# Performance work log

Measured on AMD Instinct MI355X. Metric: run time of the kernel, lower is better.

## Reference

```python
import jax, jax.numpy as jnp
import numpy as np

N = 100000      # nodes
E = 1600000     # edges (avg degree 16)
F_IN = 512      # input node features
H = 8           # heads in conv1
D = 8           # per-head dim in conv1
C = 7           # classes
NEG_SLOPE = 0.2 # PyG GATConv default leaky_relu slope


def setup_inputs() -> dict:
    key = jax.random.key(0)
    ks = jax.random.split(key, 10)
    s = 0.05
    return {
        "x": jax.random.normal(ks[0], (N, F_IN), jnp.float32),
        "edge_index": jax.random.randint(ks[1], (2, E), 0, N, dtype=jnp.int64),
        "W1": jax.random.normal(ks[2], (F_IN, H * D), jnp.float32) * s,
        "a1_src": jax.random.normal(ks[3], (H, D), jnp.float32) * s,
        "a1_dst": jax.random.normal(ks[4], (H, D), jnp.float32) * s,
        "b1": jnp.zeros((H * D,), jnp.float32),
        "W2": jax.random.normal(ks[5], (H * D, C), jnp.float32) * s,
        "a2_src": jax.random.normal(ks[6], (1, C), jnp.float32) * s,
        "a2_dst": jax.random.normal(ks[7], (1, C), jnp.float32) * s,
        "b2": jnp.zeros((C,), jnp.float32),
    }


def _gat_conv(x, src, dst, W, a_src, a_dst, b, heads, dim, concat, n):
    # linear transform -> [N, H, D]
    h = (x @ W).reshape(n, heads, dim)
    # per-node attention halves: [N, H]
    al_src = jnp.einsum('nhd,hd->nh', h, a_src)
    al_dst = jnp.einsum('nhd,hd->nh', h, a_dst)
    # per-edge logits, leaky relu: [E', H]
    e = jax.nn.leaky_relu(al_src[src] + al_dst[dst], NEG_SLOPE)
    # segment softmax over incoming edges of each dst node
    m = jax.lax.stop_gradient(jax.ops.segment_max(e, dst, num_segments=n))
    p = jnp.exp(e - m[dst])
    z = jax.ops.segment_sum(p, dst, num_segments=n)
    alpha = p / z[dst]                                   # [E', H]
    # weighted scatter-add of source messages -> [N, H, D]
    out = jax.ops.segment_sum(h[src] * alpha[..., None], dst, num_segments=n)
    out = out.reshape(n, heads * dim) if concat else out.mean(axis=1)
    return out + b


def reference(x, edge_index, W1, a1_src, a1_dst, b1, W2, a2_src, a2_dst, b2):
    n = x.shape[0]
    # PyG GATConv default: add self loops
    loops = jnp.arange(n, dtype=edge_index.dtype)
    src = jnp.concatenate([edge_index[0], loops])
    dst = jnp.concatenate([edge_index[1], loops])
    h = _gat_conv(x, src, dst, W1, a1_src, a1_dst, b1, H, D, True, n)
    h = jax.nn.elu(h)
    out = _gat_conv(h, src, dst, W2, a2_src, a2_dst, b2, 1, C, False, n)
    return jax.nn.log_softmax(out, axis=1)
```

## Files before the change

kernel.cpp:

```cpp
#include <hip/hip_runtime.h>
#include <math.h>

#define N_NODES 100000
#define N_EDGES 1600000
#define F_IN 512
#define HD 64
#define CC 7
#define NKT (F_IN / 32)
#define BS 64
#define NBK ((N_NODES + BS - 1) / BS)
#define ECAP 2048
#define SCHUNK 16384
#define SBLK ((N_EDGES + SCHUNK - 1) / SCHUNK)
#define GEMMBLKS ((N_NODES + 63) / 64)
#define W1WORK (NKT * 4 * 64)

typedef __attribute__((ext_vector_type(8))) short short8;
typedef __attribute__((ext_vector_type(4))) float f32x4;

__device__ inline unsigned short f2bf(float f) {
    union { float f; unsigned u; } v; v.f = f;
    unsigned u = v.u;
    return (unsigned short)((u + 0x7fffu + ((u >> 16) & 1u)) >> 16);
}
__device__ inline float bf2f(unsigned short b) {
    union { unsigned u; float f; } v; v.u = ((unsigned)b) << 16;
    return v.f;
}

__global__ __launch_bounds__(256) void prep_kernel(const float* __restrict__ W1,
                                                   unsigned short* __restrict__ wf,
                                                   int* __restrict__ bcur) {
    if (blockIdx.x == 16) {
        for (int i = threadIdx.x; i < NBK; i += 256) bcur[i] = 0;
        return;
    }
    int t = blockIdx.x * 256 + threadIdx.x;
    if (t >= W1WORK) return;
    int lane = t & 63;
    int ct = (t >> 6) & 3;
    int kt = t >> 8;
    int k0 = kt * 32 + (lane >> 4) * 8;
    int col = ct * 16 + (lane & 15);
    unsigned short* dst = wf + (size_t)t * 8;
    #pragma unroll
    for (int j = 0; j < 8; ++j) dst[j] = f2bf(W1[(k0 + j) * HD + col]);
}

__global__ __launch_bounds__(256) void fused_kernel(
        const int* __restrict__ ei, int* __restrict__ bcur, int* __restrict__ pairs,
        const float* __restrict__ x, const unsigned short* __restrict__ wf,
        const float* __restrict__ a1s, const float* __restrict__ a1d,
        unsigned short* __restrict__ h1b, float* __restrict__ als,
        float* __restrict__ ald) {
    __shared__ float ls[64 * 65];
    const int bid = blockIdx.x;
    const int tid = threadIdx.x;
    if (bid < SBLK) {
        int* cnt = (int*)ls;
        int* bas = cnt + NBK;
        const int e0 = bid * SCHUNK;
        int e1 = e0 + SCHUNK; if (e1 > N_EDGES) e1 = N_EDGES;
        for (int b = tid; b < NBK; b += 256) cnt[b] = 0;
        __syncthreads();
        for (int i = e0 + tid; i < e1; i += 256)
            atomicAdd(&cnt[ei[N_EDGES + i] >> 6], 1);
        __syncthreads();
        const int boff = (bid * 263) % NBK;
        for (int bb = tid; bb < NBK; bb += 256) {
            int b = bb + boff; if (b >= NBK) b -= NBK;
            int c = cnt[b];
            bas[b] = c ? atomicAdd(&bcur[b], c) : 0;
            cnt[b] = 0;
        }
        __syncthreads();
        for (int i = e0 + tid; i < e1; i += 256) {
            int s = ei[i];
            int t = ei[N_EDGES + i];
            int b = t >> 6;
            int pos = bas[b] + atomicAdd(&cnt[b], 1);
            if (pos < ECAP) pairs[(size_t)b * ECAP + pos] = (s << 6) | (t & (BS - 1));
        }
        return;
    }
    const int gb = bid - SBLK;
    const int wave = tid >> 6;
    const int lane = tid & 63;
    int arow = gb * 64 + wave * 16 + (lane & 15);
    if (arow >= N_NODES) arow = N_NODES - 1;
    const float* xp = x + (size_t)arow * F_IN + (lane >> 4) * 8;
    const short8* wp = (const short8*)wf;

    f32x4 acc[4] = {};
    #pragma unroll 4
    for (int kt = 0; kt < NKT; ++kt) {
        f32x4 a0 = *(const f32x4*)(xp + kt * 32);
        f32x4 a1 = *(const f32x4*)(xp + kt * 32 + 4);
        union { short8 s; unsigned short u[8]; } af;
        af.u[0] = f2bf(a0.x); af.u[1] = f2bf(a0.y);
        af.u[2] = f2bf(a0.z); af.u[3] = f2bf(a0.w);
        af.u[4] = f2bf(a1.x); af.u[5] = f2bf(a1.y);
        af.u[6] = f2bf(a1.z); af.u[7] = f2bf(a1.w);
        #pragma unroll
        for (int ct = 0; ct < 4; ++ct) {
            short8 bf = wp[kt * 256 + ct * 64 + lane];
            acc[ct] = __builtin_amdgcn_mfma_f32_16x16x32_bf16(af.s, bf, acc[ct], 0, 0, 0);
        }
    }
    const int lrow_base = wave * 16 + (lane >> 4) * 4;
    const int ocol = lane & 15;
    #pragma unroll
    for (int ct = 0; ct < 4; ++ct) {
        #pragma unroll
        for (int r = 0; r < 4; ++r) {
            int lrow = lrow_base + r;
            int orow = gb * 64 + lrow;
            ls[lrow * 65 + ct * 16 + ocol] = acc[ct][r];
            if (orow < N_NODES)
                h1b[(size_t)orow * HD + ct * 16 + ocol] = f2bf(acc[ct][r]);
        }
    }
    __syncthreads();
    #pragma unroll
    for (int task = tid; task < 64 * 8; task += 256) {
        int r = task >> 3, h = task & 7;
        int node = gb * 64 + r;
        if (node < N_NODES) {
            float s = 0.f, d = 0.f;
            #pragma unroll
            for (int k = 0; k < 8; ++k) {
                float v = ls[r * 65 + h * 8 + k];
                s += v * a1s[h * 8 + k];
                d += v * a1d[h * 8 + k];
            }
            als[node * 8 + h] = s;
            ald[node * 8 + h] = d;
        }
    }
}

__global__ __launch_bounds__(256) void sortcsr_kernel(const int* __restrict__ bcur,
                                                      const int* __restrict__ pairs,
                                                      int* __restrict__ csr_src,
                                                      int* __restrict__ rowptr,
                                                      int* __restrict__ rowcnt) {
    __shared__ int cnt[BS];
    __shared__ int start[BS];
    __shared__ int srcl[ECAP];
    const int tid = threadIdx.x;
    const int lane = tid & 63;
    const int n0 = blockIdx.x * BS;
    const size_t bbase = (size_t)blockIdx.x * ECAP;
    const int* bp = pairs + bbase;
    int ne = bcur[blockIdx.x]; if (ne > ECAP) ne = ECAP;
    if (tid < BS) cnt[tid] = 0;
    __syncthreads();
    for (int k = tid; k < ne; k += 256)
        atomicAdd(&cnt[bp[k] & (BS - 1)], 1);
    __syncthreads();
    if (tid < 64) {
        int a = cnt[lane];
        int xx = a;
        #pragma unroll
        for (int o = 1; o < 64; o <<= 1) { int u = __shfl_up(xx, o, 64); if (lane >= o) xx += u; }
        start[lane] = xx - a;
        cnt[lane] = 0;
    }
    __syncthreads();
    for (int k = tid; k < ne; k += 256) {
        int v = bp[k];
        int ln = v & (BS - 1);
        int pos = start[ln] + atomicAdd(&cnt[ln], 1);
        srcl[pos] = v >> 6;
    }
    __syncthreads();
    for (int k = tid; k < ne; k += 256) csr_src[bbase + k] = srcl[k];
    if (tid < BS) {
        int node = n0 + tid;
        if (node < N_NODES) {
            rowptr[node] = (int)bbase + start[tid];
            rowcnt[node] = cnt[tid];
        }
    }
}

__global__ __launch_bounds__(256) void gather1_kernel(
        const int* __restrict__ rowptr, const int* __restrict__ rowcnt,
        const int* __restrict__ csr_src,
        const float* __restrict__ als, const float* __restrict__ ald,
        const unsigned short* __restrict__ h1b, const float* __restrict__ b1,
        const float* __restrict__ W2, const float* __restrict__ a2s,
        const float* __restrict__ a2d,
        unsigned short* __restrict__ g2b, float* __restrict__ al2s,
        float* __restrict__ al2d) {
    int node = (blockIdx.x * 256 + threadIdx.x) >> 6;
    if (node >= N_NODES) return;
    const int lane = threadIdx.x & 63;
    const int h = lane >> 3;
    const int e8 = lane & 7, base8 = lane & 56;
    const int rs = rowptr[node], ncnt = rowcnt[node];
    const float aldt = ald[node * 8 + h];
    float e = als[node * 8 + h] + aldt;
    e = (e >= 0.f) ? e : 0.2f * e;
    float p = __expf(e);
    float acc = p * bf2f(h1b[(size_t)node * HD + lane]);
    float z = p;
    int k = 0;
    for (; k + 8 <= ncnt; k += 8) {
        int s_own = csr_src[rs + k + e8];
        int se[8];
        #pragma unroll
        for (int q = 0; q < 8; ++q) se[q] = __shfl(s_own, base8 | q, 64);
        float ve[8];
        #pragma unroll
        for (int q = 0; q < 8; ++q) ve[q] = bf2f(h1b[(size_t)se[q] * HD + lane]);
        float ee = als[s_own * 8 + h] + aldt;
        ee = (ee >= 0.f) ? ee : 0.2f * ee;
        float pv = __expf(ee);
        #pragma unroll
        for (int q = 0; q < 8; ++q) {
            float pe = __shfl(pv, base8 | q, 64);
            z += pe;
            acc = fmaf(pe, ve[q], acc);
        }
    }
    if (k < ncnt) {
        const int m = ncnt - k;
        int idx = rs + k + ((e8 < m) ? e8 : (m - 1));
        int s_own = csr_src[idx];
        int se[8];
        #pragma unroll
        for (int q = 0; q < 8; ++q) se[q] = __shfl(s_own, base8 | q, 64);
        float ee = als[s_own * 8 + h] + aldt;
        ee = (ee >= 0.f) ? ee : 0.2f * ee;
        float pv = __expf(ee);
        for (int q = 0; q < m; ++q) {
            float pe = __shfl(pv, base8 | q, 64);
            float ve = bf2f(h1b[(size_t)se[q] * HD + lane]);
            z += pe;
            acc = fmaf(pe, ve, acc);
        }
    }
    float v = acc / z + b1[lane];
    v = (v > 0.f) ? v : (__expf(v) - 1.f);
    float w[CC];
    #pragma unroll
    for (int c = 0; c < CC; ++c) w[c] = W2[lane * CC + c];
    float g[CC];
    #pragma unroll
    for (int c = 0; c < CC; ++c) {
        float r = v * w[c];
        #pragma unroll
        for (int d = 1; d < 64; d <<= 1) r += __shfl_xor(r, d, 64);
        g[c] = r;
    }
    float s2 = 0.f, d2 = 0.f;
    #pragma unroll
    for (int c = 0; c < CC; ++c) { s2 += g[c] * a2s[c]; d2 += g[c] * a2d[c]; }
    if (lane < CC) g2b[(size_t)node * 8 + lane] = f2bf(g[lane]);
    if (lane == CC) g2b[(size_t)node * 8 + CC] = 0;
    if (lane == 8) al2s[node] = s2;
    if (lane == 9) al2d[node] = d2;
}

__global__ __launch_bounds__(256) void gather2_kernel(
        const int* __restrict__ rowptr, const int* __restrict__ rowcnt,
        const int* __restrict__ csr_src,
        const float* __restrict__ al2s, const float* __restrict__ al2d,
        const unsigned short* __restrict__ g2b, const float* __restrict__ b2,
        float* __restrict__ out) {
    int gid = blockIdx.x * 256 + threadIdx.x;
    int n = gid >> 3, c = gid & 7;
    if (n >= N_NODES) return;
    const int lane = threadIdx.x & 63;
    const int base8 = lane & 56;
    const int rs = rowptr[n], ncnt = rowcnt[n];
    const float adn = al2d[n];
    float e = al2s[n] + adn;
    e = (e >= 0.f) ? e : 0.2f * e;
    float p = __expf(e);
    float acc = p * bf2f(g2b[(size_t)n * 8 + c]);
    float z = p;
    int k = 0;
    for (; k + 8 <= ncnt; k += 8) {
        int s_own = csr_src[rs + k + c];
        int se[8];
        #pragma unroll
        for (int q = 0; q < 8; ++q) se[q] = __shfl(s_own, base8 | q, 64);
        float ve[8];
        #pragma unroll
        for (int q = 0; q < 8; ++q) ve[q] = bf2f(g2b[(size_t)se[q] * 8 + c]);
        float ee = al2s[s_own] + adn;
        ee = (ee >= 0.f) ? ee : 0.2f * ee;
        float pv = __expf(ee);
        #pragma unroll
        for (int q = 0; q < 8; ++q) {
            float pe = __shfl(pv, base8 | q, 64);
            z += pe;
            acc = fmaf(pe, ve[q], acc);
        }
    }
    if (k < ncnt) {
        const int m = ncnt - k;
        int idx = rs + k + ((c < m) ? c : (m - 1));
        int s_own = csr_src[idx];
        int se[8];
        #pragma unroll
        for (int q = 0; q < 8; ++q) se[q] = __shfl(s_own, base8 | q, 64);
        float ee = al2s[s_own] + adn;
        ee = (ee >= 0.f) ? ee : 0.2f * ee;
        float pv = __expf(ee);
        for (int q = 0; q < m; ++q) {
            float pe = __shfl(pv, base8 | q, 64);
            float ve = bf2f(g2b[(size_t)se[q] * 8 + c]);
            z += pe;
            acc = fmaf(pe, ve, acc);
        }
    }
    float o = (c < CC) ? (acc / z + b2[c]) : -1e30f;
    float m2 = o;
    #pragma unroll
    for (int d = 1; d < 8; d <<= 1) m2 = fmaxf(m2, __shfl_xor(m2, d, 8));
    float ex = (c < CC) ? __expf(o - m2) : 0.f;
    float sum = ex;
    #pragma unroll
    for (int d = 1; d < 8; d <<= 1) sum += __shfl_xor(sum, d, 8);
    float lse = m2 + __logf(sum);
    if (c < CC) out[(size_t)n * CC + c] = o - lse;
}

extern "C" void kernel_launch(void* const* d_in, const int* in_sizes, int n_in,
                              void* d_out, int out_size, void* d_ws, size_t ws_size,
                              hipStream_t stream) {
    const float* x   = (const float*)d_in[0];
    const int*   ei  = (const int*)d_in[1];
    const float* W1  = (const float*)d_in[2];
    const float* a1s = (const float*)d_in[3];
    const float* a1d = (const float*)d_in[4];
    const float* b1  = (const float*)d_in[5];
    const float* W2  = (const float*)d_in[6];
    const float* a2s = (const float*)d_in[7];
    const float* a2d = (const float*)d_in[8];
    const float* b2  = (const float*)d_in[9];
    float* out = (float*)d_out;

    char* base = (char*)d_ws;
    size_t off = 0;
    auto alloc = [&](size_t bytes) { char* p = base + off; off = (off + bytes + 63) & ~(size_t)63; return p; };
    unsigned short* h1b = (unsigned short*)alloc((size_t)N_NODES * HD * 2);
    unsigned short* wf  = (unsigned short*)alloc((size_t)W1WORK * 8 * 2);
    float* als  = (float*)alloc((size_t)N_NODES * 8 * 4);
    float* ald  = (float*)alloc((size_t)N_NODES * 8 * 4);
    unsigned short* g2b = (unsigned short*)alloc((size_t)N_NODES * 8 * 2);
    float* al2s = (float*)alloc((size_t)N_NODES * 4);
    float* al2d = (float*)alloc((size_t)N_NODES * 4);
    int* bcur   = (int*)alloc((size_t)NBK * 4);
    int* rowptr = (int*)alloc((size_t)N_NODES * 4);
    int* rowcnt = (int*)alloc((size_t)N_NODES * 4);
    int* csr_src= (int*)alloc((size_t)NBK * ECAP * 4);
    int* pairs  = (int*)alloc((size_t)NBK * ECAP * 4);

    prep_kernel<<<17, 256, 0, stream>>>(W1, wf, bcur);
    fused_kernel<<<SBLK + GEMMBLKS, 256, 0, stream>>>(
        ei, bcur, pairs, x, wf, a1s, a1d, h1b, als, ald);
    sortcsr_kernel<<<NBK, 256, 0, stream>>>(bcur, pairs, csr_src, rowptr, rowcnt);
    gather1_kernel<<<(N_NODES * 64 + 255) / 256, 256, 0, stream>>>(
        rowptr, rowcnt, csr_src, als, ald, h1b, b1, W2, a2s, a2d, g2b, al2s, al2d);
    gather2_kernel<<<(N_NODES * 8 + 255) / 256, 256, 0, stream>>>(
        rowptr, rowcnt, csr_src, al2s, al2d, g2b, b2, out);
}
```

Baseline: 217.9 us.

## Software-pipeline neighbor gathers in layer-1 aggregation and shrink scatter chunk size

The layer-1 edge aggregation loop now prefetches the next chunk's source indices and gathered bf16 features while the current chunk is being accumulated, keeping more gather loads in flight per wave. This targets latency in the gather-bound aggregation. It raises register pressure, and the veB copy may be left uninitialized on the last iteration. Separately, SCHUNK drops from 16384 to 4096, which gives the edge-scatter/sort phase more and smaller blocks.

```diff
diff --git a/kernel.cpp b/kernel.cpp
--- a/kernel.cpp
+++ b/kernel.cpp
@@ -10,7 +10,7 @@
 #define BS 64
 #define NBK ((N_NODES + BS - 1) / BS)
 #define ECAP 2048
-#define SCHUNK 16384
+#define SCHUNK 4096
 #define SBLK ((N_EDGES + SCHUNK - 1) / SCHUNK)
 #define GEMMBLKS ((N_NODES + 63) / 64)
 #define W1WORK (NKT * 4 * 64)
@@ -205,25 +205,43 @@
     float p = __expf(e);
     float acc = p * bf2f(h1b[(size_t)node * HD + lane]);
     float z = p;
-    int k = 0;
-    for (; k + 8 <= ncnt; k += 8) {
-        int s_own = csr_src[rs + k + e8];
-        int se[8];
-        #pragma unroll
-        for (int q = 0; q < 8; ++q) se[q] = __shfl(s_own, base8 | q, 64);
-        float ve[8];
-        #pragma unroll
-        for (int q = 0; q < 8; ++q) ve[q] = bf2f(h1b[(size_t)se[q] * HD + lane]);
-        float ee = als[s_own * 8 + h] + aldt;
-        ee = (ee >= 0.f) ? ee : 0.2f * ee;
-        float pv = __expf(ee);
-        #pragma unroll
-        for (int q = 0; q < 8; ++q) {
-            float pe = __shfl(pv, base8 | q, 64);
-            z += pe;
-            acc = fmaf(pe, ve[q], acc);
-        }
-    }
+    const int nch = ncnt >> 3;
+    if (nch > 0) {
+        int sA = csr_src[rs + e8];
+        int sB = (nch > 1) ? csr_src[rs + 8 + e8] : 0;
+        float veA[8];
+        {
+            int seA[8];
+            #pragma unroll
+            for (int q = 0; q < 8; ++q) seA[q] = __shfl(sA, base8 | q, 64);
+            #pragma unroll
+            for (int q = 0; q < 8; ++q) veA[q] = bf2f(h1b[(size_t)seA[q] * HD + lane]);
+        }
+        for (int ch = 0; ch < nch; ++ch) {
+            int sC = (ch + 2 < nch) ? csr_src[rs + (ch + 2) * 8 + e8] : 0;
+            float veB[8];
+            if (ch + 1 < nch) {
+                int seB[8];
+                #pragma unroll
+                for (int q = 0; q < 8; ++q) seB[q] = __shfl(sB, base8 | q, 64);
+                #pragma unroll
+                for (int q = 0; q < 8; ++q) veB[q] = bf2f(h1b[(size_t)seB[q] * HD + lane]);
+            }
+            float ee = als[sA * 8 + h] + aldt;
+            ee = (ee >= 0.f) ? ee : 0.2f * ee;
+            float pv = __expf(ee);
+            #pragma unroll
+            for (int q = 0; q < 8; ++q) {
+                float pe = __shfl(pv, base8 | q, 64);
+                z += pe;
+                acc = fmaf(pe, veA[q], acc);
+            }
+            sA = sB; sB = sC;
+            #pragma unroll
+            for (int q = 0; q < 8; ++q) veA[q] = veB[q];
+        }
+    }
+    int k = nch << 3;
     if (k < ncnt) {
         const int m = ncnt - k;
         int idx = rs + k + ((e8 < m) ? e8 : (m - 1));
```

New measurement: 204.5 us. 1.07x faster.
